# Kernel tuning notes

Hardware: AMD Instinct MI355X
Metric: run time of the kernel (lower is better)

Reference implementation:

```python
import jax, jax.numpy as jnp
import numpy as np

N = 50000       # nodes
E = 150000      # directed edges
NODE_IN = 64
EDGE_IN = 16
D = 32          # node_out_feats
EDGE_HID = 128
STEPS = 3       # num_step_message_passing


def setup_inputs() -> dict:
    key = jax.random.key(0)
    ks = jax.random.split(key, 10)
    s = 0.05
    return {
        "x": jax.random.normal(ks[0], (N, NODE_IN), jnp.float32),
        "edge_index": jax.random.randint(ks[1], (2, E), 0, N),
        "edge_attr": jax.random.normal(ks[2], (E, EDGE_IN), jnp.float32),
        # node_init Linear
        "Wn": jax.random.normal(ks[3], (NODE_IN, D), jnp.float32) * s,
        "bn": jnp.zeros((D,), jnp.float32),
        # edge_network: Linear(edge_in, hid) -> ReLU -> Linear(hid, D*D)
        "We1": jax.random.normal(ks[4], (EDGE_IN, EDGE_HID), jnp.float32) * s,
        "be1": jnp.zeros((EDGE_HID,), jnp.float32),
        "We2": jax.random.normal(ks[5], (EDGE_HID, D * D), jnp.float32) * s,
        "be2": jnp.zeros((D * D,), jnp.float32),
        # NNConv root weight + bias
        "Wroot": jax.random.normal(ks[6], (D, D), jnp.float32) * s,
        "bconv": jnp.zeros((D,), jnp.float32),
        # GRU (gate order r, z, n as in torch)
        "Wih": jax.random.normal(ks[7], (3 * D, D), jnp.float32) * s,
        "Whh": jax.random.normal(ks[8], (3 * D, D), jnp.float32) * s,
        "bih": jnp.zeros((3 * D,), jnp.float32),
        "bhh": jnp.zeros((3 * D,), jnp.float32),
    }


def _gru_cell(xt, h, Wih, Whh, bih, bhh):
    gi = xt @ Wih.T + bih   # [N, 3D]
    gh = h @ Whh.T + bhh    # [N, 3D]
    r = jax.nn.sigmoid(gi[:, :D] + gh[:, :D])
    z = jax.nn.sigmoid(gi[:, D:2 * D] + gh[:, D:2 * D])
    n = jnp.tanh(gi[:, 2 * D:] + r * gh[:, 2 * D:])
    return (1.0 - z) * n + z * h


def reference(x, edge_index, edge_attr, Wn, bn, We1, be1, We2, be2,
              Wroot, bconv, Wih, Whh, bih, bhh):
    src, dst = edge_index[0], edge_index[1]
    # per-edge weight matrices from edge_network (edge_attr fixed across steps)
    Wm = (jax.nn.relu(edge_attr @ We1 + be1) @ We2 + be2).reshape(E, D, D)
    h = jax.nn.relu(x @ Wn + bn)   # node_init
    hid = h                        # GRU hidden state
    for _ in range(STEPS):
        # NNConv: gather -> per-edge matmul -> scatter-add, plus root + bias
        m = jnp.einsum('ei,eio->eo', h[src], Wm)                # [E, D]
        agg = jax.ops.segment_sum(m, dst, num_segments=N)       # [N, D]
        conv = jax.nn.relu(agg + h @ Wroot + bconv)
        hid = _gru_cell(conv, hid, Wih, Whh, bih, bhh)
        h = hid
    return h
```

## Files before the change

kernel.cpp:

```cpp
#include <hip/hip_runtime.h>
#include <hip/hip_bf16.h>

#define N_NODES 50000
#define N_EDGES 150000
#define NODE_IN 64
#define EDGE_IN 16
#define DD 32
#define EHID 128
#define STEPS 3
#define EPB 128

__device__ __forceinline__ ushort f2b(float f) {
    __hip_bfloat16 b = __float2bfloat16(f);
    return *reinterpret_cast<ushort*>(&b);
}

typedef __bf16 bf16x8 __attribute__((ext_vector_type(8)));
typedef float  f32x4  __attribute__((ext_vector_type(4)));

#define LDA  136
#define HPAD 36

__global__ __launch_bounds__(256) void prep(const float* __restrict__ we2,
                                            const float* __restrict__ we1,
                                            const float* __restrict__ wroot,
                                            const float* __restrict__ wih,
                                            const float* __restrict__ whh,
                                            ushort* __restrict__ we2B,
                                            ushort* __restrict__ we1B,
                                            ushort* __restrict__ wgB) {
    int i = blockIdx.x * 256 + threadIdx.x;
    if (i < 16384) {
        int l = i & 63, f = i >> 6;
        int kt = f & 3, nt = (f >> 2) & 3, bn = f >> 4;
        int lr = l & 15, lg = l >> 4;
        int n = bn * 64 + nt * 16 + lr;
        int k0 = kt * 32 + lg * 8;
        ushort tmp[8];
#pragma unroll
        for (int j = 0; j < 8; ++j) tmp[j] = f2b(we2[(size_t)(k0 + j) * 1024 + n]);
        *(uint4*)(we2B + (size_t)i * 8) = *(uint4*)tmp;
    } else if (i < 16896) {
        int u = i - 16384;
        int l = u & 63, nt = u >> 6;
        int lr = l & 15, lg = l >> 4;
        int n = nt * 16 + lr;
        ushort tmp[8];
#pragma unroll
        for (int j = 0; j < 8; ++j) {
            int k = lg * 8 + j;
            tmp[j] = (k < EDGE_IN) ? f2b(we1[(size_t)k * EHID + n]) : (ushort)0;
        }
        *(uint4*)(we1B + (size_t)u * 8) = *(uint4*)tmp;
    } else if (i < 17792) {
        int u = i - 16896;
        int l = u & 63;
        int lr = l & 15, lg = l >> 4;
        ushort tmp[8];
        if (u < 128) {
            int nt = u >> 6;
#pragma unroll
            for (int j = 0; j < 8; ++j)
                tmp[j] = f2b(wroot[(size_t)(lg * 8 + j) * DD + nt * 16 + lr]);
        } else if (u < 512) {
            int nt = (u - 128) >> 6;
#pragma unroll
            for (int j = 0; j < 8; ++j)
                tmp[j] = f2b(wih[(size_t)(nt * 16 + lr) * DD + lg * 8 + j]);
        } else {
            int nt = (u - 512) >> 6;
#pragma unroll
            for (int j = 0; j < 8; ++j)
                tmp[j] = f2b(whh[(size_t)(nt * 16 + lr) * DD + lg * 8 + j]);
        }
        *(uint4*)(wgB + (size_t)u * 8) = *(uint4*)tmp;
    }
}

__global__ __launch_bounds__(256) void node_init(const float* __restrict__ x,
                                                 const float* __restrict__ Wn,
                                                 const float* __restrict__ bn,
                                                 float* __restrict__ h) {
    __shared__ float Wns[NODE_IN * DD];
    __shared__ float bns[DD];
    int t = threadIdx.x;
    for (int i = t; i < NODE_IN * DD; i += 256) Wns[i] = Wn[i];
    if (t < DD) bns[t] = bn[t];
    __syncthreads();
    int n = blockIdx.x * 256 + t;
    if (n >= N_NODES) return;
    float xr[NODE_IN];
    const float4* xp = (const float4*)(x + (size_t)n * NODE_IN);
#pragma unroll
    for (int q = 0; q < NODE_IN / 4; ++q) *(float4*)&xr[q * 4] = xp[q];
    float out[DD];
#pragma unroll
    for (int o = 0; o < DD; ++o) {
        float s = bns[o];
#pragma unroll
        for (int i = 0; i < NODE_IN; ++i) s += xr[i] * Wns[i * DD + o];
        out[o] = fmaxf(s, 0.f);
    }
    float4* hp = (float4*)(h + (size_t)n * DD);
#pragma unroll
    for (int q = 0; q < DD / 4; ++q) hp[q] = *(float4*)&out[q * 4];
}

__global__ __launch_bounds__(256, 4) void fused_msg(const float* __restrict__ ea,
                                                    const ushort* __restrict__ we1B,
                                                    const float* __restrict__ be1,
                                                    const ushort* __restrict__ we2B,
                                                    const float* __restrict__ be2,
                                                    const int* __restrict__ ei,
                                                    const float* __restrict__ h,
                                                    float* __restrict__ agg) {
    __shared__ __attribute__((aligned(16))) ushort AsHs[EPB * LDA];
    __shared__ float b1s[EHID];
    __shared__ float be2s[DD * DD];
    float* Hs = (float*)AsHs;
    ushort* Bs = AsHs + 9216;

    int t = threadIdx.x;
    if (t < EHID) b1s[t] = be1[t];
    for (int i = t; i < DD * DD; i += 256) be2s[i] = be2[i];

    int w = t >> 6, l = t & 63;
    int lr = l & 15, lg = l >> 4;
    int e0 = blockIdx.x * EPB;

    bf16x8 afe[2];
#pragma unroll
    for (int mi = 0; mi < 2; ++mi) {
        int e = e0 + (w * 2 + mi) * 16 + lr;
        ushort tmp[8] = {0, 0, 0, 0, 0, 0, 0, 0};
        if (lg < 2 && e < N_EDGES) {
            const float4* p = (const float4*)(ea + (size_t)e * EDGE_IN + lg * 8);
            float4 a = p[0], b = p[1];
            tmp[0] = f2b(a.x); tmp[1] = f2b(a.y); tmp[2] = f2b(a.z); tmp[3] = f2b(a.w);
            tmp[4] = f2b(b.x); tmp[5] = f2b(b.y); tmp[6] = f2b(b.z); tmp[7] = f2b(b.w);
        }
        afe[mi] = *(bf16x8*)tmp;
    }
    __syncthreads();

#pragma unroll
    for (int nt = 0; nt < 8; ++nt) {
        bf16x8 bfe = *(const bf16x8*)(we1B + (size_t)((nt << 6) + l) * 8);
        int kh = nt * 16 + lr;
        float bb = b1s[kh];
#pragma unroll
        for (int mi = 0; mi < 2; ++mi) {
            f32x4 acc = (f32x4){0.f, 0.f, 0.f, 0.f};
            acc = __builtin_amdgcn_mfma_f32_16x16x32_bf16(afe[mi], bfe, acc, 0, 0, 0);
#pragma unroll
            for (int r = 0; r < 4; ++r)
                AsHs[((w * 2 + mi) * 16 + lg * 4 + r) * LDA + kh] = f2b(fmaxf(acc[r] + bb, 0.f));
        }
    }
    __syncthreads();

    bf16x8 afrag[2][4];
#pragma unroll
    for (int mi = 0; mi < 2; ++mi)
#pragma unroll
        for (int kt = 0; kt < 4; ++kt)
            afrag[mi][kt] = *(const bf16x8*)(&AsHs[((w * 2 + mi) * 16 + lr) * LDA + kt * 32 + lg * 8]);
    __syncthreads();

    {
        int row = t >> 1, half = t & 1;
        int e = e0 + row;
        float4* hd = (float4*)(Hs + row * HPAD) + half * 4;
        if (e < N_EDGES) {
            const float4* hr = (const float4*)(h + (size_t)ei[e] * DD) + half * 4;
#pragma unroll
            for (int q = 0; q < 4; ++q) hd[q] = hr[q];
        } else {
            float4 z = make_float4(0.f, 0.f, 0.f, 0.f);
#pragma unroll
            for (int q = 0; q < 4; ++q) hd[q] = z;
        }
    }
#pragma unroll
    for (int q = 0; q < 4; ++q) {
        const ushort* gsrc = we2B + (size_t)(q * 256 + t) * 8;
        ushort* ldst = Bs + (size_t)(q * 256 + w * 64) * 8;
        __builtin_amdgcn_global_load_lds(
            (const __attribute__((address_space(1))) unsigned int*)gsrc,
            (__attribute__((address_space(3))) unsigned int*)ldst, 16, 0, 0);
    }
    asm volatile("s_waitcnt vmcnt(0)" ::: "memory");
    __syncthreads();

    float m_acc[2][4][2];
#pragma unroll
    for (int mi = 0; mi < 2; ++mi)
#pragma unroll
        for (int r = 0; r < 4; ++r) { m_acc[mi][r][0] = 0.f; m_acc[mi][r][1] = 0.f; }

    for (int bn = 0; bn < 16; ++bn) {
        float bv[4];
#pragma unroll
        for (int nt = 0; nt < 4; ++nt) bv[nt] = be2s[bn * 64 + nt * 16 + lr];

        f32x4 acc[2][4];
#pragma unroll
        for (int mi = 0; mi < 2; ++mi)
#pragma unroll
            for (int nt = 0; nt < 4; ++nt) acc[mi][nt] = (f32x4){0.f, 0.f, 0.f, 0.f};

#pragma unroll
        for (int kt = 0; kt < 4; ++kt) {
            const ushort* base = Bs + (size_t)(kt * 64 + l) * 8;
            bf16x8 b0 = *(const bf16x8*)(base);
            bf16x8 b1 = *(const bf16x8*)(base + 2048);
            bf16x8 b2 = *(const bf16x8*)(base + 4096);
            bf16x8 b3 = *(const bf16x8*)(base + 6144);
#pragma unroll
            for (int mi = 0; mi < 2; ++mi) {
                acc[mi][0] = __builtin_amdgcn_mfma_f32_16x16x32_bf16(afrag[mi][kt], b0, acc[mi][0], 0, 0, 0);
                acc[mi][1] = __builtin_amdgcn_mfma_f32_16x16x32_bf16(afrag[mi][kt], b1, acc[mi][1], 0, 0, 0);
                acc[mi][2] = __builtin_amdgcn_mfma_f32_16x16x32_bf16(afrag[mi][kt], b2, acc[mi][2], 0, 0, 0);
                acc[mi][3] = __builtin_amdgcn_mfma_f32_16x16x32_bf16(afrag[mi][kt], b3, acc[mi][3], 0, 0, 0);
            }
        }

#pragma unroll
        for (int mi = 0; mi < 2; ++mi) {
#pragma unroll
            for (int r = 0; r < 4; ++r) {
                int row = (w * 2 + mi) * 16 + lg * 4 + r;
                float2 hv = *(const float2*)(Hs + row * HPAD + bn * 2);
#pragma unroll
                for (int nt = 0; nt < 4; ++nt) {
                    float hi = (nt >> 1) ? hv.y : hv.x;
                    m_acc[mi][r][nt & 1] += hi * (acc[mi][nt][r] + bv[nt]);
                }
            }
        }

        if (bn < 15) {
            __syncthreads();
#pragma unroll
            for (int q = 0; q < 4; ++q) {
                const ushort* gsrc = we2B + (size_t)(bn + 1) * 8192 + (size_t)(q * 256 + t) * 8;
                ushort* ldst = Bs + (size_t)(q * 256 + w * 64) * 8;
                __builtin_amdgcn_global_load_lds(
                    (const __attribute__((address_space(1))) unsigned int*)gsrc,
                    (__attribute__((address_space(3))) unsigned int*)ldst, 16, 0, 0);
            }
            asm volatile("s_waitcnt vmcnt(0)" ::: "memory");
            __syncthreads();
        }
    }

#pragma unroll
    for (int mi = 0; mi < 2; ++mi) {
#pragma unroll
        for (int r = 0; r < 4; ++r) {
            int le = (w * 2 + mi) * 16 + lg * 4 + r;
            int e = e0 + le;
            if (e < N_EDGES) {
                int dst = ei[N_EDGES + e];
                float* ar = agg + (size_t)dst * DD;
                atomicAdd(ar + lr,      m_acc[mi][r][0]);
                atomicAdd(ar + lr + 16, m_acc[mi][r][1]);
            }
        }
    }
}

__global__ __launch_bounds__(256) void conv_gru(float* agg,
                                                float* __restrict__ h,
                                                const ushort* __restrict__ wgB,
                                                const float* __restrict__ bconv,
                                                const float* __restrict__ bih,
                                                const float* __restrict__ bhh,
                                                float* out) {
    __shared__ __attribute__((aligned(16))) ushort Ah[64 * 40];
    __shared__ __attribute__((aligned(16))) ushort Ac[64 * 40];
    __shared__ float hs[64 * 33];
    __shared__ float bcs[DD], bis[3 * DD], bhs[3 * DD];
    int t = threadIdx.x;
    int base = blockIdx.x * 64;

    for (int idx = t; idx < 64 * DD; idx += 256) {
        int row = idx >> 5, col = idx & 31;
        int n = base + row;
        float v = (n < N_NODES) ? h[(size_t)n * DD + col] : 0.f;
        hs[row * 33 + col] = v;
        Ah[row * 40 + col] = f2b(v);
    }
    if (t < DD) bcs[t] = bconv[t];
    if (t < 3 * DD) { bis[t] = bih[t]; bhs[t] = bhh[t]; }
    __syncthreads();

    int w = t >> 6, l = t & 63;
    int lr = l & 15, lg = l >> 4;
    const f32x4 zro = (f32x4){0.f, 0.f, 0.f, 0.f};

    bf16x8 ah = *(const bf16x8*)(&Ah[(w * 16 + lr) * 40 + lg * 8]);

    f32x4 dcv[2];
#pragma unroll
    for (int nt = 0; nt < 2; ++nt) {
        bf16x8 b = *(const bf16x8*)(wgB + (size_t)(nt * 64 + l) * 8);
        dcv[nt] = __builtin_amdgcn_mfma_f32_16x16x32_bf16(ah, b, zro, 0, 0, 0);
    }
#pragma unroll
    for (int nt = 0; nt < 2; ++nt) {
#pragma unroll
        for (int r = 0; r < 4; ++r) {
            int row = w * 16 + lg * 4 + r;
            int col = nt * 16 + lr;
            int n = base + row;
            float a = 0.f;
            if (n < N_NODES) {
                a = agg[(size_t)n * DD + col];
                agg[(size_t)n * DD + col] = 0.f;
            }
            Ac[row * 40 + col] = f2b(fmaxf(dcv[nt][r] + a + bcs[col], 0.f));
        }
    }
    __syncthreads();

    bf16x8 ac = *(const bf16x8*)(&Ac[(w * 16 + lr) * 40 + lg * 8]);

    f32x4 gi[6], gh[6];
#pragma unroll
    for (int nt = 0; nt < 6; ++nt) {
        bf16x8 bi_ = *(const bf16x8*)(wgB + (size_t)(128 + nt * 64 + l) * 8);
        gi[nt] = __builtin_amdgcn_mfma_f32_16x16x32_bf16(ac, bi_, zro, 0, 0, 0);
        bf16x8 bh_ = *(const bf16x8*)(wgB + (size_t)(512 + nt * 64 + l) * 8);
        gh[nt] = __builtin_amdgcn_mfma_f32_16x16x32_bf16(ah, bh_, zro, 0, 0, 0);
    }

#pragma unroll
    for (int r = 0; r < 4; ++r) {
        int row = w * 16 + lg * 4 + r;
        int n = base + row;
        if (n >= N_NODES) continue;
#pragma unroll
        for (int ch = 0; ch < 2; ++ch) {
            int o = ch * 16 + lr;
            float girv = gi[ch][r]     + bis[o];
            float gizv = gi[2 + ch][r] + bis[DD + o];
            float ginv = gi[4 + ch][r] + bis[2 * DD + o];
            float ghrv = gh[ch][r]     + bhs[o];
            float ghzv = gh[2 + ch][r] + bhs[DD + o];
            float ghnv = gh[4 + ch][r] + bhs[2 * DD + o];
            float R  = 1.f / (1.f + expf(-(girv + ghrv)));
            float Z  = 1.f / (1.f + expf(-(gizv + ghzv)));
            float Nn = tanhf(ginv + R * ghnv);
            float hold = hs[row * 33 + o];
            float hnew = (1.f - Z) * Nn + Z * hold;
            h[(size_t)n * DD + o] = hnew;
            if (out) out[(size_t)n * DD + o] = hnew;
        }
    }
}

extern "C" void kernel_launch(void* const* d_in, const int* in_sizes, int n_in,
                              void* d_out, int out_size, void* d_ws, size_t ws_size,
                              hipStream_t stream) {
    const float* x    = (const float*)d_in[0];
    const int*   ei   = (const int*)d_in[1];
    const float* ea   = (const float*)d_in[2];
    const float* Wn   = (const float*)d_in[3];
    const float* bn   = (const float*)d_in[4];
    const float* We1  = (const float*)d_in[5];
    const float* be1  = (const float*)d_in[6];
    const float* We2  = (const float*)d_in[7];
    const float* be2  = (const float*)d_in[8];
    const float* Wroot= (const float*)d_in[9];
    const float* bconv= (const float*)d_in[10];
    const float* Wih  = (const float*)d_in[11];
    const float* Whh  = (const float*)d_in[12];
    const float* bih  = (const float*)d_in[13];
    const float* bhh  = (const float*)d_in[14];
    float* out = (float*)d_out;

    char* ws = (char*)d_ws;
    float*  h    = (float*)(ws);
    ushort* we2B = (ushort*)(ws + 6400000);
    ushort* we1B = (ushort*)(ws + 6662144);
    ushort* wgB  = (ushort*)(ws + 6670336);
    float*  agg  = (float*)d_out;

    prep<<<70, 256, 0, stream>>>(We2, We1, Wroot, Wih, Whh, we2B, we1B, wgB);
    node_init<<<(N_NODES + 255) / 256, 256, 0, stream>>>(x, Wn, bn, h);
    hipMemsetAsync(agg, 0, (size_t)N_NODES * DD * sizeof(float), stream);

    for (int step = 0; step < STEPS; ++step) {
        fused_msg<<<(N_EDGES + EPB - 1) / EPB, 256, 0, stream>>>(ea, we1B, be1, we2B, be2,
                                                                 ei, h, agg);
        conv_gru<<<(N_NODES + 63) / 64, 256, 0, stream>>>(agg, h, wgB, bconv, bih, bhh,
                                                          (step == STEPS - 1) ? out : nullptr);
    }
}
```

Baseline: 334.8 us.

## Replace atomic scatter-add with CSR gather of bf16 per-edge messages

Builds a CSR index of edges grouped by destination once per call (histogram, three-pass scan, fill) and changes fused_msg to write per-edge messages as bf16 to a workspace buffer instead of doing float atomics into agg. conv_gru then gathers and sums each node's incoming messages through the permutation, which removes the agg memset and atomic traffic and lets h live directly in the output buffer. In exchange it adds several small setup launches, a 9.6MB message write/read per step, irregular per-node loops with divergence, and bf16 rounding of messages before summation.

Result: slower. 356.7 us (+6.5%).

```diff
diff --git a/kernel.cpp b/kernel.cpp
--- a/kernel.cpp
+++ b/kernel.cpp
@@ -9,17 +9,23 @@
 #define EHID 128
 #define STEPS 3
 #define EPB 128
+#define NSCAN 196
 
 __device__ __forceinline__ ushort f2b(float f) {
     __hip_bfloat16 b = __float2bfloat16(f);
     return *reinterpret_cast<ushort*>(&b);
 }
+__device__ __forceinline__ float b2f(ushort u) {
+    unsigned int x = ((unsigned int)u) << 16;
+    return __uint_as_float(x);
+}
 
 typedef __bf16 bf16x8 __attribute__((ext_vector_type(8)));
 typedef float  f32x4  __attribute__((ext_vector_type(4)));
 
 #define LDA  136
 #define HPAD 36
+#define MPAD 40
 
 __global__ __launch_bounds__(256) void prep(const float* __restrict__ we2,
                                             const float* __restrict__ we1,
@@ -77,6 +83,82 @@
     }
 }
 
+__global__ __launch_bounds__(256) void hist(const int* __restrict__ ei,
+                                            int* __restrict__ cnt) {
+    int e = blockIdx.x * 256 + threadIdx.x;
+    if (e < N_EDGES) atomicAdd(&cnt[ei[N_EDGES + e]], 1);
+}
+
+__global__ __launch_bounds__(256) void scan1(int* __restrict__ cnt,
+                                             int* __restrict__ bsum) {
+    __shared__ int wsum[4];
+    int b = blockIdx.x, t = threadIdx.x;
+    int lane = t & 63, wid = t >> 6;
+    int i = b * 256 + t;
+    int v = (i < N_NODES) ? cnt[i] : 0;
+    int s = v;
+#pragma unroll
+    for (int off = 1; off < 64; off <<= 1) {
+        int u = __shfl_up(s, off);
+        if (lane >= off) s += u;
+    }
+    if (lane == 63) wsum[wid] = s;
+    __syncthreads();
+    if (t == 0) {
+        int a = 0;
+#pragma unroll
+        for (int k = 0; k < 4; ++k) { int tmp = wsum[k]; wsum[k] = a; a += tmp; }
+    }
+    __syncthreads();
+    int excl = s - v + wsum[wid];
+    if (i < N_NODES) cnt[i] = excl;
+    if (t == 255) bsum[b] = excl + v;
+}
+
+__global__ __launch_bounds__(256) void scan2(int* __restrict__ bsum) {
+    __shared__ int wsum[4];
+    int t = threadIdx.x;
+    int lane = t & 63, wid = t >> 6;
+    int v = (t < NSCAN) ? bsum[t] : 0;
+    int s = v;
+#pragma unroll
+    for (int off = 1; off < 64; off <<= 1) {
+        int u = __shfl_up(s, off);
+        if (lane >= off) s += u;
+    }
+    if (lane == 63) wsum[wid] = s;
+    __syncthreads();
+    if (t == 0) {
+        int a = 0;
+#pragma unroll
+        for (int k = 0; k < 4; ++k) { int tmp = wsum[k]; wsum[k] = a; a += tmp; }
+    }
+    __syncthreads();
+    if (t < NSCAN) bsum[t] = s - v + wsum[wid];
+}
+
+__global__ __launch_bounds__(256) void scan3(const int* __restrict__ cnt,
+                                             const int* __restrict__ bsum,
+                                             int* __restrict__ off,
+                                             int* __restrict__ cur) {
+    int i = blockIdx.x * 256 + threadIdx.x;
+    if (i < N_NODES) {
+        int o = cnt[i] + bsum[blockIdx.x];
+        off[i] = o;
+        cur[i] = o;
+    }
+}
+
+__global__ __launch_bounds__(256) void scatter_fill(const int* __restrict__ ei,
+                                                    int* __restrict__ cur,
+                                                    int* __restrict__ perm) {
+    int e = blockIdx.x * 256 + threadIdx.x;
+    if (e >= N_EDGES) return;
+    int d = ei[N_EDGES + e];
+    int pos = atomicAdd(&cur[d], 1);
+    perm[pos] = e;
+}
+
 __global__ __launch_bounds__(256) void node_init(const float* __restrict__ x,
                                                  const float* __restrict__ Wn,
                                                  const float* __restrict__ bn,
@@ -113,12 +195,13 @@
                                                     const float* __restrict__ be2,
                                                     const int* __restrict__ ei,
                                                     const float* __restrict__ h,
-                                                    float* __restrict__ agg) {
+                                                    ushort* __restrict__ msg) {
     __shared__ __attribute__((aligned(16))) ushort AsHs[EPB * LDA];
     __shared__ float b1s[EHID];
     __shared__ float be2s[DD * DD];
     float* Hs = (float*)AsHs;
     ushort* Bs = AsHs + 9216;
+    ushort* Ms = AsHs;
 
     int t = threadIdx.x;
     if (t < EHID) b1s[t] = be1[t];
@@ -254,29 +337,37 @@
         }
     }
 
+    __syncthreads();
 #pragma unroll
     for (int mi = 0; mi < 2; ++mi) {
 #pragma unroll
         for (int r = 0; r < 4; ++r) {
-            int le = (w * 2 + mi) * 16 + lg * 4 + r;
-            int e = e0 + le;
-            if (e < N_EDGES) {
-                int dst = ei[N_EDGES + e];
-                float* ar = agg + (size_t)dst * DD;
-                atomicAdd(ar + lr,      m_acc[mi][r][0]);
-                atomicAdd(ar + lr + 16, m_acc[mi][r][1]);
-            }
-        }
-    }
-}
-
-__global__ __launch_bounds__(256) void conv_gru(float* agg,
+            int row = (w * 2 + mi) * 16 + lg * 4 + r;
+            Ms[row * MPAD + lr]      = f2b(m_acc[mi][r][0]);
+            Ms[row * MPAD + lr + 16] = f2b(m_acc[mi][r][1]);
+        }
+    }
+    __syncthreads();
+    {
+        int row = t >> 1, half = t & 1;
+        int e = e0 + row;
+        if (e < N_EDGES) {
+            const uint4* src = (const uint4*)(Ms + row * MPAD);
+            uint4* dst = (uint4*)(msg + (size_t)e * DD);
+            dst[half * 2]     = src[half * 2];
+            dst[half * 2 + 1] = src[half * 2 + 1];
+        }
+    }
+}
+
+__global__ __launch_bounds__(256) void conv_gru(const ushort* __restrict__ msg,
+                                                const int* __restrict__ perm,
+                                                const int* __restrict__ off,
                                                 float* __restrict__ h,
                                                 const ushort* __restrict__ wgB,
                                                 const float* __restrict__ bconv,
                                                 const float* __restrict__ bih,
-                                                const float* __restrict__ bhh,
-                                                float* out) {
+                                                const float* __restrict__ bhh) {
     __shared__ __attribute__((aligned(16))) ushort Ah[64 * 40];
     __shared__ __attribute__((aligned(16))) ushort Ac[64 * 40];
     __shared__ float hs[64 * 33];
@@ -308,19 +399,22 @@
         dcv[nt] = __builtin_amdgcn_mfma_f32_16x16x32_bf16(ah, b, zro, 0, 0, 0);
     }
 #pragma unroll
-    for (int nt = 0; nt < 2; ++nt) {
-#pragma unroll
-        for (int r = 0; r < 4; ++r) {
-            int row = w * 16 + lg * 4 + r;
-            int col = nt * 16 + lr;
-            int n = base + row;
-            float a = 0.f;
-            if (n < N_NODES) {
-                a = agg[(size_t)n * DD + col];
-                agg[(size_t)n * DD + col] = 0.f;
+    for (int r = 0; r < 4; ++r) {
+        int row = w * 16 + lg * 4 + r;
+        int n = base + row;
+        float a0 = 0.f, a1 = 0.f;
+        if (n < N_NODES) {
+            int beg = off[n];
+            int end = (n + 1 < N_NODES) ? off[n + 1] : N_EDGES;
+            for (int j = beg; j < end; ++j) {
+                int e = perm[j];
+                const ushort* mr = msg + (size_t)e * DD;
+                a0 += b2f(mr[lr]);
+                a1 += b2f(mr[lr + 16]);
             }
-            Ac[row * 40 + col] = f2b(fmaxf(dcv[nt][r] + a + bcs[col], 0.f));
-        }
+        }
+        Ac[row * 40 + lr]      = f2b(fmaxf(dcv[0][r] + a0 + bcs[lr], 0.f));
+        Ac[row * 40 + lr + 16] = f2b(fmaxf(dcv[1][r] + a1 + bcs[lr + 16], 0.f));
     }
     __syncthreads();
 
@@ -355,7 +449,6 @@
             float hold = hs[row * 33 + o];
             float hnew = (1.f - Z) * Nn + Z * hold;
             h[(size_t)n * DD + o] = hnew;
-            if (out) out[(size_t)n * DD + o] = hnew;
         }
     }
 }
@@ -378,23 +471,32 @@
     const float* Whh  = (const float*)d_in[12];
     const float* bih  = (const float*)d_in[13];
     const float* bhh  = (const float*)d_in[14];
-    float* out = (float*)d_out;
 
     char* ws = (char*)d_ws;
-    float*  h    = (float*)(ws);
-    ushort* we2B = (ushort*)(ws + 6400000);
-    ushort* we1B = (ushort*)(ws + 6662144);
-    ushort* wgB  = (ushort*)(ws + 6670336);
-    float*  agg  = (float*)d_out;
-
+    ushort* msg  = (ushort*)(ws);
+    ushort* we2B = (ushort*)(ws + 9600000);
+    ushort* we1B = (ushort*)(ws + 9862144);
+    ushort* wgB  = (ushort*)(ws + 9870336);
+    int*    cnt  = (int*)(ws + 9884672);
+    int*    off  = (int*)(ws + 10084672);
+    int*    cur  = (int*)(ws + 10284672);
+    int*    perm = (int*)(ws + 10484672);
+    int*    bsum = (int*)(ws + 11084672);
+    float*  h    = (float*)d_out;
+
+    hipMemsetAsync(cnt, 0, (size_t)N_NODES * sizeof(int), stream);
     prep<<<70, 256, 0, stream>>>(We2, We1, Wroot, Wih, Whh, we2B, we1B, wgB);
     node_init<<<(N_NODES + 255) / 256, 256, 0, stream>>>(x, Wn, bn, h);
-    hipMemsetAsync(agg, 0, (size_t)N_NODES * DD * sizeof(float), stream);
+    hist<<<(N_EDGES + 255) / 256, 256, 0, stream>>>(ei, cnt);
+    scan1<<<NSCAN, 256, 0, stream>>>(cnt, bsum);
+    scan2<<<1, 256, 0, stream>>>(bsum);
+    scan3<<<NSCAN, 256, 0, stream>>>(cnt, bsum, off, cur);
+    scatter_fill<<<(N_EDGES + 255) / 256, 256, 0, stream>>>(ei, cur, perm);
 
     for (int step = 0; step < STEPS; ++step) {
         fused_msg<<<(N_EDGES + EPB - 1) / EPB, 256, 0, stream>>>(ea, we1B, be1, we2B, be2,
-                                                                 ei, h, agg);
-        conv_gru<<<(N_NODES + 63) / 64, 256, 0, stream>>>(agg, h, wgB, bconv, bih, bhh,
-                                                          (step == STEPS - 1) ? out : nullptr);
-    }
-}
+                                                                 ei, h, msg);
+        conv_gru<<<(N_NODES + 63) / 64, 256, 0, stream>>>(msg, perm, off, h, wgB,
+                                                          bconv, bih, bhh);
+    }
+}
```

## Halve edges per block in message kernel and merge prep with node init

Applied to the files above, without the earlier changes.

Cuts the edges handled per fused_msg block from 128 to 64, giving one 16-row MFMA tile per wave instead of two, and shrinks shared memory so more blocks fit per CU (launch bound raised to 5). The weight-prep and node-init kernels are merged into one launch to save a kernel dispatch. The trade-off is that the bf16 We2 tiles are reloaded from global memory for every block, so with half as many edges per block that weight traffic doubles.

Result: faster. 318.2 us (-5.0%).

```diff
diff --git a/kernel.cpp b/kernel.cpp
--- a/kernel.cpp
+++ b/kernel.cpp
@@ -8,7 +8,7 @@
 #define DD 32
 #define EHID 128
 #define STEPS 3
-#define EPB 128
+#define EPB 64
 
 __device__ __forceinline__ ushort f2b(float f) {
     __hip_bfloat16 b = __float2bfloat16(f);
@@ -21,92 +21,94 @@
 #define LDA  136
 #define HPAD 36
 
-__global__ __launch_bounds__(256) void prep(const float* __restrict__ we2,
-                                            const float* __restrict__ we1,
-                                            const float* __restrict__ wroot,
-                                            const float* __restrict__ wih,
-                                            const float* __restrict__ whh,
-                                            ushort* __restrict__ we2B,
-                                            ushort* __restrict__ we1B,
-                                            ushort* __restrict__ wgB) {
-    int i = blockIdx.x * 256 + threadIdx.x;
-    if (i < 16384) {
-        int l = i & 63, f = i >> 6;
-        int kt = f & 3, nt = (f >> 2) & 3, bn = f >> 4;
-        int lr = l & 15, lg = l >> 4;
-        int n = bn * 64 + nt * 16 + lr;
-        int k0 = kt * 32 + lg * 8;
-        ushort tmp[8];
-#pragma unroll
-        for (int j = 0; j < 8; ++j) tmp[j] = f2b(we2[(size_t)(k0 + j) * 1024 + n]);
-        *(uint4*)(we2B + (size_t)i * 8) = *(uint4*)tmp;
-    } else if (i < 16896) {
-        int u = i - 16384;
-        int l = u & 63, nt = u >> 6;
-        int lr = l & 15, lg = l >> 4;
-        int n = nt * 16 + lr;
-        ushort tmp[8];
-#pragma unroll
-        for (int j = 0; j < 8; ++j) {
-            int k = lg * 8 + j;
-            tmp[j] = (k < EDGE_IN) ? f2b(we1[(size_t)k * EHID + n]) : (ushort)0;
-        }
-        *(uint4*)(we1B + (size_t)u * 8) = *(uint4*)tmp;
-    } else if (i < 17792) {
-        int u = i - 16896;
-        int l = u & 63;
-        int lr = l & 15, lg = l >> 4;
-        ushort tmp[8];
-        if (u < 128) {
-            int nt = u >> 6;
-#pragma unroll
-            for (int j = 0; j < 8; ++j)
-                tmp[j] = f2b(wroot[(size_t)(lg * 8 + j) * DD + nt * 16 + lr]);
-        } else if (u < 512) {
-            int nt = (u - 128) >> 6;
-#pragma unroll
-            for (int j = 0; j < 8; ++j)
-                tmp[j] = f2b(wih[(size_t)(nt * 16 + lr) * DD + lg * 8 + j]);
-        } else {
-            int nt = (u - 512) >> 6;
-#pragma unroll
-            for (int j = 0; j < 8; ++j)
-                tmp[j] = f2b(whh[(size_t)(nt * 16 + lr) * DD + lg * 8 + j]);
-        }
-        *(uint4*)(wgB + (size_t)u * 8) = *(uint4*)tmp;
-    }
-}
-
-__global__ __launch_bounds__(256) void node_init(const float* __restrict__ x,
-                                                 const float* __restrict__ Wn,
-                                                 const float* __restrict__ bn,
-                                                 float* __restrict__ h) {
+__global__ __launch_bounds__(256) void setup(const float* __restrict__ we2,
+                                             const float* __restrict__ we1,
+                                             const float* __restrict__ wroot,
+                                             const float* __restrict__ wih,
+                                             const float* __restrict__ whh,
+                                             ushort* __restrict__ we2B,
+                                             ushort* __restrict__ we1B,
+                                             ushort* __restrict__ wgB,
+                                             const float* __restrict__ x,
+                                             const float* __restrict__ Wn,
+                                             const float* __restrict__ bn,
+                                             float* __restrict__ h) {
     __shared__ float Wns[NODE_IN * DD];
     __shared__ float bns[DD];
-    int t = threadIdx.x;
-    for (int i = t; i < NODE_IN * DD; i += 256) Wns[i] = Wn[i];
-    if (t < DD) bns[t] = bn[t];
-    __syncthreads();
-    int n = blockIdx.x * 256 + t;
-    if (n >= N_NODES) return;
-    float xr[NODE_IN];
-    const float4* xp = (const float4*)(x + (size_t)n * NODE_IN);
-#pragma unroll
-    for (int q = 0; q < NODE_IN / 4; ++q) *(float4*)&xr[q * 4] = xp[q];
-    float out[DD];
-#pragma unroll
-    for (int o = 0; o < DD; ++o) {
-        float s = bns[o];
-#pragma unroll
-        for (int i = 0; i < NODE_IN; ++i) s += xr[i] * Wns[i * DD + o];
-        out[o] = fmaxf(s, 0.f);
-    }
-    float4* hp = (float4*)(h + (size_t)n * DD);
-#pragma unroll
-    for (int q = 0; q < DD / 4; ++q) hp[q] = *(float4*)&out[q * 4];
-}
-
-__global__ __launch_bounds__(256, 4) void fused_msg(const float* __restrict__ ea,
+    int b = blockIdx.x, t = threadIdx.x;
+
+    if (b < 70) {
+        int i = b * 256 + t;
+        if (i < 16384) {
+            int l = i & 63, f = i >> 6;
+            int kt = f & 3, nt = (f >> 2) & 3, bq = f >> 4;
+            int lr = l & 15, lg = l >> 4;
+            int n = bq * 64 + nt * 16 + lr;
+            int k0 = kt * 32 + lg * 8;
+            ushort tmp[8];
+#pragma unroll
+            for (int j = 0; j < 8; ++j) tmp[j] = f2b(we2[(size_t)(k0 + j) * 1024 + n]);
+            *(uint4*)(we2B + (size_t)i * 8) = *(uint4*)tmp;
+        } else if (i < 16896) {
+            int u = i - 16384;
+            int l = u & 63, nt = u >> 6;
+            int lr = l & 15, lg = l >> 4;
+            int n = nt * 16 + lr;
+            ushort tmp[8];
+#pragma unroll
+            for (int j = 0; j < 8; ++j) {
+                int k = lg * 8 + j;
+                tmp[j] = (k < EDGE_IN) ? f2b(we1[(size_t)k * EHID + n]) : (ushort)0;
+            }
+            *(uint4*)(we1B + (size_t)u * 8) = *(uint4*)tmp;
+        } else if (i < 17792) {
+            int u = i - 16896;
+            int l = u & 63;
+            int lr = l & 15, lg = l >> 4;
+            ushort tmp[8];
+            if (u < 128) {
+                int nt = u >> 6;
+#pragma unroll
+                for (int j = 0; j < 8; ++j)
+                    tmp[j] = f2b(wroot[(size_t)(lg * 8 + j) * DD + nt * 16 + lr]);
+            } else if (u < 512) {
+                int nt = (u - 128) >> 6;
+#pragma unroll
+                for (int j = 0; j < 8; ++j)
+                    tmp[j] = f2b(wih[(size_t)(nt * 16 + lr) * DD + lg * 8 + j]);
+            } else {
+                int nt = (u - 512) >> 6;
+#pragma unroll
+                for (int j = 0; j < 8; ++j)
+                    tmp[j] = f2b(whh[(size_t)(nt * 16 + lr) * DD + lg * 8 + j]);
+            }
+            *(uint4*)(wgB + (size_t)u * 8) = *(uint4*)tmp;
+        }
+    } else {
+        for (int i = t; i < NODE_IN * DD; i += 256) Wns[i] = Wn[i];
+        if (t < DD) bns[t] = bn[t];
+        __syncthreads();
+        int n = (b - 70) * 256 + t;
+        if (n >= N_NODES) return;
+        float xr[NODE_IN];
+        const float4* xp = (const float4*)(x + (size_t)n * NODE_IN);
+#pragma unroll
+        for (int q = 0; q < NODE_IN / 4; ++q) *(float4*)&xr[q * 4] = xp[q];
+        float out[DD];
+#pragma unroll
+        for (int o = 0; o < DD; ++o) {
+            float s = bns[o];
+#pragma unroll
+            for (int i = 0; i < NODE_IN; ++i) s += xr[i] * Wns[i * DD + o];
+            out[o] = fmaxf(s, 0.f);
+        }
+        float4* hp = (float4*)(h + (size_t)n * DD);
+#pragma unroll
+        for (int q = 0; q < DD / 4; ++q) hp[q] = *(float4*)&out[q * 4];
+    }
+}
+
+__global__ __launch_bounds__(256, 5) void fused_msg(const float* __restrict__ ea,
                                                     const ushort* __restrict__ we1B,
                                                     const float* __restrict__ be1,
                                                     const ushort* __restrict__ we2B,
@@ -114,11 +116,11 @@
                                                     const int* __restrict__ ei,
                                                     const float* __restrict__ h,
                                                     float* __restrict__ agg) {
-    __shared__ __attribute__((aligned(16))) ushort AsHs[EPB * LDA];
+    __shared__ __attribute__((aligned(16))) ushort AsHs[12800];
     __shared__ float b1s[EHID];
     __shared__ float be2s[DD * DD];
     float* Hs = (float*)AsHs;
-    ushort* Bs = AsHs + 9216;
+    ushort* Bs = AsHs + 4608;
 
     int t = threadIdx.x;
     if (t < EHID) b1s[t] = be1[t];
@@ -128,10 +130,9 @@
     int lr = l & 15, lg = l >> 4;
     int e0 = blockIdx.x * EPB;
 
-    bf16x8 afe[2];
-#pragma unroll
-    for (int mi = 0; mi < 2; ++mi) {
-        int e = e0 + (w * 2 + mi) * 16 + lr;
+    bf16x8 afe;
+    {
+        int e = e0 + w * 16 + lr;
         ushort tmp[8] = {0, 0, 0, 0, 0, 0, 0, 0};
         if (lg < 2 && e < N_EDGES) {
             const float4* p = (const float4*)(ea + (size_t)e * EDGE_IN + lg * 8);
@@ -139,7 +140,7 @@
             tmp[0] = f2b(a.x); tmp[1] = f2b(a.y); tmp[2] = f2b(a.z); tmp[3] = f2b(a.w);
             tmp[4] = f2b(b.x); tmp[5] = f2b(b.y); tmp[6] = f2b(b.z); tmp[7] = f2b(b.w);
         }
-        afe[mi] = *(bf16x8*)tmp;
+        afe = *(bf16x8*)tmp;
     }
     __syncthreads();
 
@@ -148,37 +149,31 @@
         bf16x8 bfe = *(const bf16x8*)(we1B + (size_t)((nt << 6) + l) * 8);
         int kh = nt * 16 + lr;
         float bb = b1s[kh];
-#pragma unroll
-        for (int mi = 0; mi < 2; ++mi) {
-            f32x4 acc = (f32x4){0.f, 0.f, 0.f, 0.f};
-            acc = __builtin_amdgcn_mfma_f32_16x16x32_bf16(afe[mi], bfe, acc, 0, 0, 0);
-#pragma unroll
-            for (int r = 0; r < 4; ++r)
-                AsHs[((w * 2 + mi) * 16 + lg * 4 + r) * LDA + kh] = f2b(fmaxf(acc[r] + bb, 0.f));
-        }
-    }
-    __syncthreads();
-
-    bf16x8 afrag[2][4];
-#pragma unroll
-    for (int mi = 0; mi < 2; ++mi)
-#pragma unroll
-        for (int kt = 0; kt < 4; ++kt)
-            afrag[mi][kt] = *(const bf16x8*)(&AsHs[((w * 2 + mi) * 16 + lr) * LDA + kt * 32 + lg * 8]);
+        f32x4 acc = (f32x4){0.f, 0.f, 0.f, 0.f};
+        acc = __builtin_amdgcn_mfma_f32_16x16x32_bf16(afe, bfe, acc, 0, 0, 0);
+#pragma unroll
+        for (int r = 0; r < 4; ++r)
+            AsHs[(w * 16 + lg * 4 + r) * LDA + kh] = f2b(fmaxf(acc[r] + bb, 0.f));
+    }
+    __syncthreads();
+
+    bf16x8 afrag[4];
+#pragma unroll
+    for (int kt = 0; kt < 4; ++kt)
+        afrag[kt] = *(const bf16x8*)(&AsHs[(w * 16 + lr) * LDA + kt * 32 + lg * 8]);
     __syncthreads();
 
     {
-        int row = t >> 1, half = t & 1;
+        int row = t >> 2, qtr = t & 3;
         int e = e0 + row;
-        float4* hd = (float4*)(Hs + row * HPAD) + half * 4;
+        float4* hd = (float4*)(Hs + row * HPAD) + qtr * 2;
         if (e < N_EDGES) {
-            const float4* hr = (const float4*)(h + (size_t)ei[e] * DD) + half * 4;
-#pragma unroll
-            for (int q = 0; q < 4; ++q) hd[q] = hr[q];
+            const float4* hr = (const float4*)(h + (size_t)ei[e] * DD) + qtr * 2;
+            hd[0] = hr[0];
+            hd[1] = hr[1];
         } else {
             float4 z = make_float4(0.f, 0.f, 0.f, 0.f);
-#pragma unroll
-            for (int q = 0; q < 4; ++q) hd[q] = z;
+            hd[0] = z; hd[1] = z;
         }
     }
 #pragma unroll
@@ -192,22 +187,18 @@
     asm volatile("s_waitcnt vmcnt(0)" ::: "memory");
     __syncthreads();
 
-    float m_acc[2][4][2];
-#pragma unroll
-    for (int mi = 0; mi < 2; ++mi)
-#pragma unroll
-        for (int r = 0; r < 4; ++r) { m_acc[mi][r][0] = 0.f; m_acc[mi][r][1] = 0.f; }
+    float m_acc[4][2];
+#pragma unroll
+    for (int r = 0; r < 4; ++r) { m_acc[r][0] = 0.f; m_acc[r][1] = 0.f; }
 
     for (int bn = 0; bn < 16; ++bn) {
         float bv[4];
 #pragma unroll
         for (int nt = 0; nt < 4; ++nt) bv[nt] = be2s[bn * 64 + nt * 16 + lr];
 
-        f32x4 acc[2][4];
-#pragma unroll
-        for (int mi = 0; mi < 2; ++mi)
-#pragma unroll
-            for (int nt = 0; nt < 4; ++nt) acc[mi][nt] = (f32x4){0.f, 0.f, 0.f, 0.f};
+        f32x4 acc[4];
+#pragma unroll
+        for (int nt = 0; nt < 4; ++nt) acc[nt] = (f32x4){0.f, 0.f, 0.f, 0.f};
 
 #pragma unroll
         for (int kt = 0; kt < 4; ++kt) {
@@ -216,26 +207,20 @@
             bf16x8 b1 = *(const bf16x8*)(base + 2048);
             bf16x8 b2 = *(const bf16x8*)(base + 4096);
             bf16x8 b3 = *(const bf16x8*)(base + 6144);
-#pragma unroll
-            for (int mi = 0; mi < 2; ++mi) {
-                acc[mi][0] = __builtin_amdgcn_mfma_f32_16x16x32_bf16(afrag[mi][kt], b0, acc[mi][0], 0, 0, 0);
-                acc[mi][1] = __builtin_amdgcn_mfma_f32_16x16x32_bf16(afrag[mi][kt], b1, acc[mi][1], 0, 0, 0);
-                acc[mi][2] = __builtin_amdgcn_mfma_f32_16x16x32_bf16(afrag[mi][kt], b2, acc[mi][2], 0, 0, 0);
-                acc[mi][3] = __builtin_amdgcn_mfma_f32_16x16x32_bf16(afrag[mi][kt], b3, acc[mi][3], 0, 0, 0);
-            }
-        }
-
-#pragma unroll
-        for (int mi = 0; mi < 2; ++mi) {
-#pragma unroll
-            for (int r = 0; r < 4; ++r) {
-                int row = (w * 2 + mi) * 16 + lg * 4 + r;
-                float2 hv = *(const float2*)(Hs + row * HPAD + bn * 2);
-#pragma unroll
-                for (int nt = 0; nt < 4; ++nt) {
-                    float hi = (nt >> 1) ? hv.y : hv.x;
-                    m_acc[mi][r][nt & 1] += hi * (acc[mi][nt][r] + bv[nt]);
-                }
+            acc[0] = __builtin_amdgcn_mfma_f32_16x16x32_bf16(afrag[kt], b0, acc[0], 0, 0, 0);
+            acc[1] = __builtin_amdgcn_mfma_f32_16x16x32_bf16(afrag[kt], b1, acc[1], 0, 0, 0);
+            acc[2] = __builtin_amdgcn_mfma_f32_16x16x32_bf16(afrag[kt], b2, acc[2], 0, 0, 0);
+            acc[3] = __builtin_amdgcn_mfma_f32_16x16x32_bf16(afrag[kt], b3, acc[3], 0, 0, 0);
+        }
+
+#pragma unroll
+        for (int r = 0; r < 4; ++r) {
+            int row = w * 16 + lg * 4 + r;
+            float2 hv = *(const float2*)(Hs + row * HPAD + bn * 2);
+#pragma unroll
+            for (int nt = 0; nt < 4; ++nt) {
+                float hi = (nt >> 1) ? hv.y : hv.x;
+                m_acc[r][nt & 1] += hi * (acc[nt][r] + bv[nt]);
             }
         }
 
@@ -255,17 +240,14 @@
     }
 
 #pragma unroll
-    for (int mi = 0; mi < 2; ++mi) {
-#pragma unroll
-        for (int r = 0; r < 4; ++r) {
-            int le = (w * 2 + mi) * 16 + lg * 4 + r;
-            int e = e0 + le;
-            if (e < N_EDGES) {
-                int dst = ei[N_EDGES + e];
-                float* ar = agg + (size_t)dst * DD;
-                atomicAdd(ar + lr,      m_acc[mi][r][0]);
-                atomicAdd(ar + lr + 16, m_acc[mi][r][1]);
-            }
+    for (int r = 0; r < 4; ++r) {
+        int le = w * 16 + lg * 4 + r;
+        int e = e0 + le;
+        if (e < N_EDGES) {
+            int dst = ei[N_EDGES + e];
+            float* ar = agg + (size_t)dst * DD;
+            atomicAdd(ar + lr,      m_acc[r][0]);
+            atomicAdd(ar + lr + 16, m_acc[r][1]);
         }
     }
 }
@@ -387,8 +369,8 @@
     ushort* wgB  = (ushort*)(ws + 6670336);
     float*  agg  = (float*)d_out;
 
-    prep<<<70, 256, 0, stream>>>(We2, We1, Wroot, Wih, Whh, we2B, we1B, wgB);
-    node_init<<<(N_NODES + 255) / 256, 256, 0, stream>>>(x, Wn, bn, h);
+    setup<<<266, 256, 0, stream>>>(We2, We1, Wroot, Wih, Whh, we2B, we1B, wgB,
+                                   x, Wn, bn, h);
     hipMemsetAsync(agg, 0, (size_t)N_NODES * DD * sizeof(float), stream);
 
     for (int step = 0; step < STEPS; ++step) {
```
